# Optimization experiments

Hardware: AMD Instinct MI355X
Metric: run time of the kernel (lower is better)

The kernel has to match this reference:

```python
import jax, jax.numpy as jnp
import numpy as np

N, E, IN_DIM, HID, OUT = 50000, 800000, 256, 128, 128
EPS_BN = 1e-5
EPS_NORM = 1e-12


def leaky(x):
    return jnp.where(x >= 0, x, 0.2 * x)


def batchnorm(x, gamma, beta):
    # training-mode BatchNorm1d over node dimension
    mean = jnp.mean(x, axis=0)
    var = jnp.var(x, axis=0)
    return gamma * (x - mean) * jax.lax.rsqrt(var + EPS_BN) + beta


def sage_conv(x, src, dst, W_l, b_l, W_r):
    # PyG SAGEConv (mean aggr): lin_l(mean_{j->i} x_j) + lin_r(x_i)
    msg = x[src]  # [E, D] gather
    agg = jax.ops.segment_sum(msg, dst, num_segments=N)
    cnt = jax.ops.segment_sum(jnp.ones((E,), x.dtype), dst, num_segments=N)
    agg = agg / jnp.maximum(cnt, 1.0)[:, None]
    return agg @ W_l + b_l + x @ W_r


def setup_inputs() -> dict:
    key = jax.random.key(0)
    ks = jax.random.split(key, 16)
    s = lambda fan_in: (2.0 / fan_in) ** 0.5
    return {
        "x": jax.random.normal(ks[0], (N, IN_DIM), jnp.float32),
        "edge_index": jax.random.randint(ks[1], (2, E), 0, N),
        "W_in": jax.random.normal(ks[2], (IN_DIM, HID), jnp.float32) * s(IN_DIM),
        "b_in": jnp.zeros((HID,), jnp.float32),
        "g1": jnp.ones((HID,), jnp.float32),
        "be1": jnp.zeros((HID,), jnp.float32),
        "Wl1": jax.random.normal(ks[3], (HID, HID), jnp.float32) * s(HID),
        "bl1": jnp.zeros((HID,), jnp.float32),
        "Wr1": jax.random.normal(ks[4], (HID, HID), jnp.float32) * s(HID),
        "Wl2": jax.random.normal(ks[5], (HID, OUT), jnp.float32) * s(HID),
        "bl2": jnp.zeros((OUT,), jnp.float32),
        "Wr2": jax.random.normal(ks[6], (HID, OUT), jnp.float32) * s(HID),
        "Wskip": jax.random.normal(ks[7], (HID, OUT), jnp.float32) * s(HID),
        "bskip": jnp.zeros((OUT,), jnp.float32),
        "g2": jnp.ones((OUT,), jnp.float32),
        "be2": jnp.zeros((OUT,), jnp.float32),
    }


def reference(x, edge_index, W_in, b_in, g1, be1, Wl1, bl1, Wr1, Wl2, bl2, Wr2, Wskip, bskip, g2, be2):
    src, dst = edge_index[0], edge_index[1]
    h = batchnorm(leaky(x @ W_in + b_in), g1, be1)
    skip = h
    h1 = leaky(sage_conv(h, src, dst, Wl1, bl1, Wr1))  # dropout = identity (eval)
    h2 = sage_conv(h1, src, dst, Wl2, bl2, Wr2)
    out = h2 + (skip @ Wskip + bskip)
    out = batchnorm(out, g2, be2)
    norm = jnp.sqrt(jnp.sum(out * out, axis=1, keepdims=True))
    return out / jnp.maximum(norm, EPS_NORM)
```

## Files before the change

### kernel.cpp

```cpp
#include <hip/hip_runtime.h>
#include <math.h>

#define N_NODES 50000
#define N_EDGES 800000
#define IN_DIM 256
#define HID 128
#define ZPITCH 384

typedef unsigned short u16;
typedef u16 u16x8 __attribute__((ext_vector_type(8)));
typedef u16 u16x2 __attribute__((ext_vector_type(2)));
typedef __bf16 bf16x8 __attribute__((ext_vector_type(8)));
typedef float f32x4 __attribute__((ext_vector_type(4)));

union F8 { u16x8 u; bf16x8 h; };

__device__ __forceinline__ u16 f2b(float f) {
    unsigned u = __builtin_bit_cast(unsigned, f);
    u = (u + 0x7FFFu + ((u >> 16) & 1u)) >> 16;
    return (u16)u;
}
__device__ __forceinline__ float b2f(u16 h) {
    unsigned u = ((unsigned)h) << 16;
    return __builtin_bit_cast(float, u);
}

template<int A_F32>
__device__ __forceinline__ F8 load_a(const void* base, size_t row, int P, int koff)
{
    F8 r;
    if (A_F32) {
        const float* p = (const float*)base + row * P + koff;
        float4 f0 = *reinterpret_cast<const float4*>(p);
        float4 f1 = *reinterpret_cast<const float4*>(p + 4);
        r.h[0] = (__bf16)f0.x; r.h[1] = (__bf16)f0.y;
        r.h[2] = (__bf16)f0.z; r.h[3] = (__bf16)f0.w;
        r.h[4] = (__bf16)f1.x; r.h[5] = (__bf16)f1.y;
        r.h[6] = (__bf16)f1.z; r.h[7] = (__bf16)f1.w;
    } else {
        r.u = *reinterpret_cast<const u16x8*>((const u16*)base + row * P + koff);
    }
    return r;
}

template<int LEAKY, int STATS, int OUT_BF16, int A_F32, int NC>
__global__ __launch_bounds__(512, 3) void gemm_mfma(
    int M, const void* __restrict__ A, int P,
    const u16* __restrict__ Wf,
    const float* __restrict__ bias0, const float* __restrict__ bias1,
    void* __restrict__ Cout, int CP,
    float* __restrict__ stats)
{
    __shared__ u16 Bs[NC * 4096];

    const int t   = threadIdx.x;
    const int w   = t >> 6;
    const int l   = t & 63;
    const int l15 = l & 15;
    const int lg  = l >> 4;
    const int rb  = blockIdx.x * 128 + w * 16;

    int r0 = rb + l15;
    size_t r0c = (size_t)(r0 < M ? r0 : M - 1);
    const int ko = lg * 8;

    F8 a[NC];
#pragma unroll
    for (int c = 0; c < NC; ++c) a[c] = load_a<A_F32>(A, r0c, P, c * 32 + ko);

#pragma unroll
    for (int i = 0; i < NC; ++i) {
        int idx = i * 512 + t;
        reinterpret_cast<u16x8*>(Bs)[idx] = reinterpret_cast<const u16x8*>(Wf)[idx];
    }
    __syncthreads();

    f32x4 acc[8];
#pragma unroll
    for (int j = 0; j < 8; ++j) acc[j] = 0.0f;

#pragma unroll
    for (int c = 0; c < NC; ++c) {
#pragma unroll
        for (int j = 0; j < 8; ++j) {
            F8 b;
            b.u = reinterpret_cast<const u16x8*>(Bs)[(c * 8 + j) * 64 + l];
            acc[j] = __builtin_amdgcn_mfma_f32_16x16x32_bf16(a[c].h, b.h, acc[j], 0, 0, 0);
        }
    }

    float bias_j[8];
#pragma unroll
    for (int j = 0; j < 8; ++j) {
        float bb = bias0[16 * j + l15];
        if (bias1) bb += bias1[16 * j + l15];
        bias_j[j] = bb;
    }

    float csum[8], csq[8];
#pragma unroll
    for (int j = 0; j < 8; ++j) { csum[j] = 0.f; csq[j] = 0.f; }

    {
        int rbase = rb + lg * 4;
#pragma unroll
        for (int r = 0; r < 4; ++r) {
            int row = rbase + r;
            bool ok = row < M;
#pragma unroll
            for (int j = 0; j < 8; ++j) {
                float y = acc[j][r] + bias_j[j];
                if (LEAKY) y = (y >= 0.f) ? y : 0.2f * y;
                if (ok) {
                    if (OUT_BF16)
                        ((u16*)Cout)[(size_t)row * CP + 16 * j + l15] = f2b(y);
                    else
                        ((float*)Cout)[(size_t)row * CP + 16 * j + l15] = y;
                    if (STATS) { csum[j] += y; csq[j] += y * y; }
                }
            }
        }
    }

    if (STATS) {
        __shared__ float sred[256];
        if (t < 256) sred[t] = 0.f;
        __syncthreads();
#pragma unroll
        for (int j = 0; j < 8; ++j) {
            float s = csum[j];
            float q = csq[j];
            s += __shfl_xor(s, 16); s += __shfl_xor(s, 32);
            q += __shfl_xor(q, 16); q += __shfl_xor(q, 32);
            if (lg == 0) {
                atomicAdd(&sred[16 * j + l15], s);
                atomicAdd(&sred[128 + 16 * j + l15], q);
            }
        }
        __syncthreads();
        if (t < 256) atomicAdd(&stats[t], sred[t]);
    }
}

__global__ __launch_bounds__(256) void conv_w(const float* s0, const float* s1, const float* s2,
                                              const float* sc0, const float* sc1, const float* sc2,
                                              int rows_each, u16* __restrict__ dst, int nchunks)
{
    int tid = blockIdx.x * 256 + threadIdx.x;
    if (tid >= nchunks * 512) return;
    int c   = tid >> 9;
    int j   = (tid >> 6) & 7;
    int l   = tid & 63;
    int l15 = l & 15, lg = l >> 4;

    int srow0 = c * 32;
    int si    = srow0 / rows_each;
    const float* S  = (si == 0) ? s0 : (si == 1) ? s1 : s2;
    const float* SC = (si == 0) ? sc0 : (si == 1) ? sc1 : sc2;
    int rbase = srow0 - si * rows_each + lg * 8;
    int col   = 16 * j + l15;

    u16x8 o;
#pragma unroll
    for (int i = 0; i < 8; ++i) {
        float v = S[(size_t)(rbase + i) * HID + col];
        if (SC) v *= SC[rbase + i];
        o[i] = f2b(v);
    }
    reinterpret_cast<u16x8*>(dst)[tid] = o;
}

__global__ void bias_fold(const float* __restrict__ b0, const float* __restrict__ b1,
                          const float* __restrict__ W0, const float* __restrict__ W1,
                          const float* __restrict__ sh, float* __restrict__ outb)
{
    int j = threadIdx.x;
    float acc = b0[j] + (b1 ? b1[j] : 0.f);
    for (int i = 0; i < HID; ++i) {
        float w = W0[(size_t)i * HID + j] + (W1 ? W1[(size_t)i * HID + j] : 0.f);
        acc = fmaf(sh[i], w, acc);
    }
    outb[j] = acc;
}

__global__ void bn_params(const float* __restrict__ stats,
                          const float* __restrict__ gamma,
                          const float* __restrict__ beta,
                          float* __restrict__ scale,
                          float* __restrict__ shift, float invn)
{
    int j = threadIdx.x;
    float mean = stats[j] * invn;
    float var  = stats[128 + j] * invn - mean * mean;
    var = fmaxf(var, 0.f);
    float sc = gamma[j] / sqrtf(var + 1e-5f);
    scale[j] = sc;
    shift[j] = beta[j] - mean * sc;
}

__global__ __launch_bounds__(256) void edge_count(const int* __restrict__ dst, int* __restrict__ cnt)
{
    int e = blockIdx.x * 256 + threadIdx.x;
    if (e < N_EDGES) atomicAdd(&cnt[dst[e]], 1);
}

__global__ __launch_bounds__(256) void scan_block(const int* __restrict__ cnt,
                                                  int* __restrict__ excl,
                                                  int* __restrict__ bsum, int n)
{
    __shared__ int sh[256];
    int t = threadIdx.x;
    int i = blockIdx.x * 256 + t;
    int v = (i < n) ? cnt[i] : 0;
    sh[t] = v;
    __syncthreads();
#pragma unroll
    for (int off = 1; off < 256; off <<= 1) {
        int x = (t >= off) ? sh[t - off] : 0;
        __syncthreads();
        sh[t] += x;
        __syncthreads();
    }
    if (i < n) excl[i] = sh[t] - v;
    if (t == 255) bsum[blockIdx.x] = sh[255];
}

__global__ __launch_bounds__(256) void scan_bsum(int* __restrict__ bsum, int nb)
{
    __shared__ int sh[256];
    int t = threadIdx.x;
    int v = (t < nb) ? bsum[t] : 0;
    sh[t] = v;
    __syncthreads();
#pragma unroll
    for (int off = 1; off < 256; off <<= 1) {
        int x = (t >= off) ? sh[t - off] : 0;
        __syncthreads();
        sh[t] += x;
        __syncthreads();
    }
    if (t < nb) bsum[t] = sh[t] - v;
}

__global__ __launch_bounds__(256) void scan_add(int* __restrict__ row_ptr,
                                                int* __restrict__ fillrp,
                                                const int* __restrict__ bsum, int n)
{
    int i = blockIdx.x * 256 + threadIdx.x;
    if (i < n) {
        int v = row_ptr[i] + bsum[i >> 8];
        row_ptr[i] = v;
        fillrp[i]  = v;
    }
    if (i == 0) row_ptr[n] = N_EDGES;
}

#define FILL_EPB 4096
__global__ __launch_bounds__(256) void edge_fill_part(const int* __restrict__ src,
                                                      const int* __restrict__ dst,
                                                      int* __restrict__ fillrp,
                                                      int* __restrict__ col_idx)
{
    const int range = blockIdx.x & 7;
    const int base  = (blockIdx.x >> 3) * FILL_EPB;
    const int lo = range * 6250, hi = lo + 6250;
#pragma unroll
    for (int k = 0; k < FILL_EPB / 256; ++k) {
        int e = base + k * 256 + threadIdx.x;
        if (e < N_EDGES) {
            int d = dst[e];
            if (d >= lo && d < hi) {
                int pos = atomicAdd(&fillrp[d], 1);
                col_idx[pos] = src[e];
            }
        }
    }
}

__global__ __launch_bounds__(256) void spmm_mean(const int* __restrict__ row_ptr,
                                                 const int* __restrict__ col_idx,
                                                 const u16* __restrict__ Z_in,
                                                 u16* __restrict__ Z_out)
{
    int node = blockIdx.x * 4 + (threadIdx.x >> 6);
    if (node >= N_NODES) return;
    int lane = threadIdx.x & 63;
    int beg = row_ptr[node];
    int end = row_ptr[node + 1];

    float sx = 0.f, sy = 0.f;
    int e = beg;
    for (; e + 4 <= end; e += 4) {
        int c0 = col_idx[e], c1 = col_idx[e + 1], c2 = col_idx[e + 2], c3 = col_idx[e + 3];
        u16x2 v0 = *reinterpret_cast<const u16x2*>(Z_in + (size_t)c0 * ZPITCH + lane * 2);
        u16x2 v1 = *reinterpret_cast<const u16x2*>(Z_in + (size_t)c1 * ZPITCH + lane * 2);
        u16x2 v2 = *reinterpret_cast<const u16x2*>(Z_in + (size_t)c2 * ZPITCH + lane * 2);
        u16x2 v3 = *reinterpret_cast<const u16x2*>(Z_in + (size_t)c3 * ZPITCH + lane * 2);
        sx += (b2f(v0[0]) + b2f(v1[0])) + (b2f(v2[0]) + b2f(v3[0]));
        sy += (b2f(v0[1]) + b2f(v1[1])) + (b2f(v2[1]) + b2f(v3[1]));
    }
    for (; e < end; ++e) {
        int c = col_idx[e];
        u16x2 v = *reinterpret_cast<const u16x2*>(Z_in + (size_t)c * ZPITCH + lane * 2);
        sx += b2f(v[0]); sy += b2f(v[1]);
    }
    float inv = 1.f / fmaxf((float)(end - beg), 1.f);
    u16x2 r; r[0] = f2b(sx * inv); r[1] = f2b(sy * inv);
    *reinterpret_cast<u16x2*>(Z_out + (size_t)node * ZPITCH + lane * 2) = r;
}

__global__ __launch_bounds__(256) void bn_rownorm(float* __restrict__ out,
                                                  const float* __restrict__ scale,
                                                  const float* __restrict__ shift)
{
    int row = blockIdx.x * 4 + (threadIdx.x >> 6);
    if (row >= N_NODES) return;
    int lane = threadIdx.x & 63;
    float2 v  = *reinterpret_cast<const float2*>(&out[(size_t)row * HID + lane * 2]);
    float2 sc = *reinterpret_cast<const float2*>(&scale[lane * 2]);
    float2 sh = *reinterpret_cast<const float2*>(&shift[lane * 2]);
    float y0 = v.x * sc.x + sh.x;
    float y1 = v.y * sc.y + sh.y;
    float ss = y0 * y0 + y1 * y1;
#pragma unroll
    for (int m = 1; m < 64; m <<= 1) ss += __shfl_xor(ss, m);
    float inv = 1.f / fmaxf(sqrtf(ss), 1e-12f);
    float2 r = {y0 * inv, y1 * inv};
    *reinterpret_cast<float2*>(&out[(size_t)row * HID + lane * 2]) = r;
}

extern "C" void kernel_launch(void* const* d_in, const int* in_sizes, int n_in,
                              void* d_out, int out_size, void* d_ws, size_t ws_size,
                              hipStream_t stream)
{
    const float* x     = (const float*)d_in[0];
    const int*   ei    = (const int*)d_in[1];
    const float* W_in  = (const float*)d_in[2];
    const float* b_in  = (const float*)d_in[3];
    const float* g1    = (const float*)d_in[4];
    const float* be1   = (const float*)d_in[5];
    const float* Wl1   = (const float*)d_in[6];
    const float* bl1   = (const float*)d_in[7];
    const float* Wr1   = (const float*)d_in[8];
    const float* Wl2   = (const float*)d_in[9];
    const float* bl2   = (const float*)d_in[10];
    const float* Wr2   = (const float*)d_in[11];
    const float* Wskip = (const float*)d_in[12];
    const float* bskip = (const float*)d_in[13];
    const float* g2    = (const float*)d_in[14];
    const float* be2   = (const float*)d_in[15];
    float* out = (float*)d_out;

    char* ws = (char*)d_ws;
    u16*  Z  = (u16*)ws;
    char* zzone = ws + 38400000;
    float* stats = (float*)zzone;
    int*   icnt  = (int*)(zzone + 2048);
    size_t zsz   = 2048 + (size_t)N_NODES * 4;
    int*   row_ptr = (int*)(zzone + zsz);
    int*   fillrp  = (int*)(zzone + zsz + 200064);
    int*   bsum    = (int*)(zzone + zsz + 400128);
    int*   col_idx = (int*)(zzone + zsz + 400128 + 1024);
    float* bnc     = (float*)(zzone + zsz + 400128 + 1024 + (size_t)N_EDGES * 4);
    u16* WfA = (u16*)((char*)bnc + 4096);
    u16* WfB = WfA + 8 * 4096;
    u16* WfC = WfB + 8 * 4096;

    hipMemsetAsync(zzone, 0, zsz, stream);

    const int* srcp = ei;
    const int* dstp = ei + N_EDGES;

    float* scale1 = bnc;
    float* shift1 = bnc + 128;
    float* scale2 = bnc + 256;
    float* shift2 = bnc + 384;
    float* b1eff  = bnc + 512;
    float* b2eff  = bnc + 640;

    conv_w<<<16, 256, 0, stream>>>(W_in, nullptr, nullptr, nullptr, nullptr, nullptr,
                                   256, WfA, 8);

    const int NB = (N_NODES + 255) / 256;
    edge_count<<<(N_EDGES + 255) / 256, 256, 0, stream>>>(dstp, icnt);
    scan_block<<<NB, 256, 0, stream>>>(icnt, row_ptr, bsum, N_NODES);
    scan_bsum<<<1, 256, 0, stream>>>(bsum, NB);
    scan_add<<<NB, 256, 0, stream>>>(row_ptr, fillrp, bsum, N_NODES);
    edge_fill_part<<<((N_EDGES + FILL_EPB - 1) / FILL_EPB) * 8, 256, 0, stream>>>(
        srcp, dstp, fillrp, col_idx);

    const int GB = (N_NODES + 127) / 128;

    gemm_mfma<1, 1, 1, 1, 8><<<GB, 512, 0, stream>>>(
        N_NODES, x, IN_DIM, WfA, b_in, nullptr, Z + 128, ZPITCH, stats);
    bn_params<<<1, 128, 0, stream>>>(stats, g1, be1, scale1, shift1, 1.f / N_NODES);

    conv_w<<<16, 256, 0, stream>>>(Wl1, Wr1, nullptr, scale1, scale1, nullptr,
                                   128, WfB, 8);
    conv_w<<<24, 256, 0, stream>>>(Wl2, Wskip, Wr2, nullptr, scale1, nullptr,
                                   128, WfC, 12);
    bias_fold<<<1, 128, 0, stream>>>(bl1, nullptr, Wl1, Wr1, shift1, b1eff);
    bias_fold<<<1, 128, 0, stream>>>(bl2, bskip, Wskip, nullptr, shift1, b2eff);

    spmm_mean<<<(N_NODES + 3) / 4, 256, 0, stream>>>(row_ptr, col_idx, Z + 128, Z);
    gemm_mfma<1, 0, 1, 0, 8><<<GB, 512, 0, stream>>>(
        N_NODES, Z, ZPITCH, WfB, b1eff, nullptr, Z + 256, ZPITCH, nullptr);

    spmm_mean<<<(N_NODES + 3) / 4, 256, 0, stream>>>(row_ptr, col_idx, Z + 256, Z);
    gemm_mfma<0, 1, 0, 0, 12><<<GB, 512, 0, stream>>>(
        N_NODES, Z, ZPITCH, WfC, b2eff, nullptr, out, HID, stats + 256);

    bn_params<<<1, 128, 0, stream>>>(stats + 256, g2, be2, scale2, shift2, 1.f / N_NODES);
    bn_rownorm<<<(N_NODES + 3) / 4, 256, 0, stream>>>(out, scale2, shift2);
}
```

Before: 276.2 us.

## Fuse mean aggregation into SAGE GEMM kernels and restructure the launch pipeline

Replaces the separate spmm_mean plus gemm passes with sage_k kernels that gather neighbour means into LDS and immediately run the MFMA GEMM, so the aggregated features are never written to global memory. It also merges weight conversion with edge counting, applies BN1 explicitly to H instead of folding it into the weights and biases, and folds BN2 parameter computation into the row-norm kernel. The first GEMM now computes two 16-row tiles per wave and uses global_load_lds for weight staging. The cost is large 1024-thread blocks with heavy LDS use, which limits occupancy for the latency-bound gather, plus an extra bn_apply pass over H.

```diff
diff --git a/kernel.cpp b/kernel.cpp
--- a/kernel.cpp
+++ b/kernel.cpp
@@ -5,7 +5,7 @@
 #define N_EDGES 800000
 #define IN_DIM 256
 #define HID 128
-#define ZPITCH 384
+#define NTILE 196
 
 typedef unsigned short u16;
 typedef u16 u16x8 __attribute__((ext_vector_type(8)));
@@ -13,6 +13,9 @@
 typedef __bf16 bf16x8 __attribute__((ext_vector_type(8)));
 typedef float f32x4 __attribute__((ext_vector_type(4)));
 
+#define AS1 __attribute__((address_space(1)))
+#define AS3 __attribute__((address_space(3)))
+
 union F8 { u16x8 u; bf16x8 h; };
 
 __device__ __forceinline__ u16 f2b(float f) {
@@ -25,67 +28,342 @@
     return __builtin_bit_cast(float, u);
 }
 
-template<int A_F32>
-__device__ __forceinline__ F8 load_a(const void* base, size_t row, int P, int koff)
-{
-    F8 r;
-    if (A_F32) {
-        const float* p = (const float*)base + row * P + koff;
-        float4 f0 = *reinterpret_cast<const float4*>(p);
-        float4 f1 = *reinterpret_cast<const float4*>(p + 4);
-        r.h[0] = (__bf16)f0.x; r.h[1] = (__bf16)f0.y;
-        r.h[2] = (__bf16)f0.z; r.h[3] = (__bf16)f0.w;
-        r.h[4] = (__bf16)f1.x; r.h[5] = (__bf16)f1.y;
-        r.h[6] = (__bf16)f1.z; r.h[7] = (__bf16)f1.w;
+__device__ __forceinline__ void conv_seg(int tid, const float* s0, const float* s1,
+                                         const float* s2, int rows_each, u16* dst)
+{
+    int c   = tid >> 9;
+    int j   = (tid >> 6) & 7;
+    int l   = tid & 63;
+    int l15 = l & 15, lg = l >> 4;
+    int srow0 = c * 32;
+    int si    = srow0 / rows_each;
+    const float* S = (si == 0) ? s0 : (si == 1) ? s1 : s2;
+    int rbase = srow0 - si * rows_each + lg * 8;
+    int col   = 16 * j + l15;
+    u16x8 o;
+#pragma unroll
+    for (int i = 0; i < 8; ++i) o[i] = f2b(S[(size_t)(rbase + i) * HID + col]);
+    reinterpret_cast<u16x8*>(dst)[tid] = o;
+}
+
+__global__ __launch_bounds__(256) void convcnt_k(
+    const float* W_in, const float* Wl1, const float* Wr1,
+    const float* Wl2, const float* Wskip, const float* Wr2,
+    u16* WfA, u16* WfB, u16* WfC,
+    const int* __restrict__ dst, int* __restrict__ icnt)
+{
+    int b = blockIdx.x;
+    if (b < 56) {
+        int tid = b * 256 + threadIdx.x;
+        if (tid < 4096)      conv_seg(tid,        W_in, nullptr, nullptr, 256, WfA);
+        else if (tid < 8192) conv_seg(tid - 4096, Wl1,  Wr1,     nullptr, 128, WfB);
+        else                 conv_seg(tid - 8192, Wl2,  Wskip,   Wr2,     128, WfC);
     } else {
-        r.u = *reinterpret_cast<const u16x8*>((const u16*)base + row * P + koff);
-    }
-    return r;
-}
-
-template<int LEAKY, int STATS, int OUT_BF16, int A_F32, int NC>
-__global__ __launch_bounds__(512, 3) void gemm_mfma(
-    int M, const void* __restrict__ A, int P,
-    const u16* __restrict__ Wf,
-    const float* __restrict__ bias0, const float* __restrict__ bias1,
-    void* __restrict__ Cout, int CP,
+        int e = (b - 56) * 256 + threadIdx.x;
+        if (e < N_EDGES) atomicAdd(&icnt[dst[e]], 1);
+    }
+}
+
+__global__ __launch_bounds__(256) void scan_block(const int* __restrict__ cnt,
+                                                  int* __restrict__ excl,
+                                                  int* __restrict__ bsum, int n)
+{
+    __shared__ int sh[256];
+    int t = threadIdx.x;
+    int i = blockIdx.x * 256 + t;
+    int v = (i < n) ? cnt[i] : 0;
+    sh[t] = v;
+    __syncthreads();
+#pragma unroll
+    for (int off = 1; off < 256; off <<= 1) {
+        int x = (t >= off) ? sh[t - off] : 0;
+        __syncthreads();
+        sh[t] += x;
+        __syncthreads();
+    }
+    if (i < n) excl[i] = sh[t] - v;
+    if (t == 255) bsum[blockIdx.x] = sh[255];
+}
+
+__global__ __launch_bounds__(256) void scan_bsum(int* __restrict__ bsum, int nb)
+{
+    __shared__ int sh[256];
+    int t = threadIdx.x;
+    int v = (t < nb) ? bsum[t] : 0;
+    sh[t] = v;
+    __syncthreads();
+#pragma unroll
+    for (int off = 1; off < 256; off <<= 1) {
+        int x = (t >= off) ? sh[t - off] : 0;
+        __syncthreads();
+        sh[t] += x;
+        __syncthreads();
+    }
+    if (t < nb) bsum[t] = sh[t] - v;
+}
+
+__global__ __launch_bounds__(256) void scan_add(int* __restrict__ row_ptr,
+                                                int* __restrict__ fillrp,
+                                                const int* __restrict__ bsum, int n)
+{
+    int i = blockIdx.x * 256 + threadIdx.x;
+    if (i < n) {
+        int v = row_ptr[i] + bsum[i >> 8];
+        row_ptr[i] = v;
+        fillrp[i]  = v;
+    }
+    if (i == 0) row_ptr[n] = N_EDGES;
+}
+
+#define FILL_EPB 4096
+__global__ __launch_bounds__(256) void edge_fill_part(const int* __restrict__ src,
+                                                      const int* __restrict__ dst,
+                                                      int* __restrict__ fillrp,
+                                                      int* __restrict__ col_idx)
+{
+    const int range = blockIdx.x & 7;
+    const int base  = (blockIdx.x >> 3) * FILL_EPB;
+    const int lo = range * 6250, hi = lo + 6250;
+#pragma unroll
+    for (int k = 0; k < FILL_EPB / 256; ++k) {
+        int e = base + k * 256 + threadIdx.x;
+        if (e < N_EDGES) {
+            int d = dst[e];
+            if (d >= lo && d < hi) {
+                int pos = atomicAdd(&fillrp[d], 1);
+                col_idx[pos] = src[e];
+            }
+        }
+    }
+}
+
+__global__ __launch_bounds__(512, 2) void gemm0_k(
+    const float* __restrict__ x, const u16* __restrict__ Wf,
+    const float* __restrict__ bias, u16* __restrict__ H,
     float* __restrict__ stats)
 {
-    __shared__ u16 Bs[NC * 4096];
-
-    const int t   = threadIdx.x;
-    const int w   = t >> 6;
-    const int l   = t & 63;
-    const int l15 = l & 15;
-    const int lg  = l >> 4;
-    const int rb  = blockIdx.x * 128 + w * 16;
-
-    int r0 = rb + l15;
-    size_t r0c = (size_t)(r0 < M ? r0 : M - 1);
+    __shared__ u16 Bs[8 * 4096];
+    __shared__ float sred[256];
+    const int t = threadIdx.x, w = t >> 6, l = t & 63, l15 = l & 15, lg = l >> 4;
+    const int rb = blockIdx.x * 256 + w * 32;
+    const int r0 = rb + l15, r1 = r0 + 16;
+    const size_t r0c = (size_t)(r0 < N_NODES ? r0 : N_NODES - 1);
+    const size_t r1c = (size_t)(r1 < N_NODES ? r1 : N_NODES - 1);
     const int ko = lg * 8;
 
-    F8 a[NC];
-#pragma unroll
-    for (int c = 0; c < NC; ++c) a[c] = load_a<A_F32>(A, r0c, P, c * 32 + ko);
-
-#pragma unroll
-    for (int i = 0; i < NC; ++i) {
+#pragma unroll
+    for (int i = 0; i < 8; ++i) {
         int idx = i * 512 + t;
-        reinterpret_cast<u16x8*>(Bs)[idx] = reinterpret_cast<const u16x8*>(Wf)[idx];
-    }
-    __syncthreads();
-
-    f32x4 acc[8];
-#pragma unroll
-    for (int j = 0; j < 8; ++j) acc[j] = 0.0f;
-
-#pragma unroll
-    for (int c = 0; c < NC; ++c) {
+        __builtin_amdgcn_global_load_lds((const AS1 void*)(Wf + (size_t)idx * 8),
+                                         (AS3 void*)(Bs + (size_t)idx * 8), 16, 0, 0);
+    }
+    __syncthreads();
+
+    f32x4 acc[2][8];
+#pragma unroll
+    for (int m = 0; m < 2; ++m)
+#pragma unroll
+        for (int j = 0; j < 8; ++j) acc[m][j] = 0.0f;
+
+#pragma unroll
+    for (int c = 0; c < 8; ++c) {
+        F8 fa0, fa1;
+        {
+            const float* p = x + r0c * IN_DIM + c * 32 + ko;
+            float4 f0 = *reinterpret_cast<const float4*>(p);
+            float4 f1 = *reinterpret_cast<const float4*>(p + 4);
+            fa0.h[0] = (__bf16)f0.x; fa0.h[1] = (__bf16)f0.y;
+            fa0.h[2] = (__bf16)f0.z; fa0.h[3] = (__bf16)f0.w;
+            fa0.h[4] = (__bf16)f1.x; fa0.h[5] = (__bf16)f1.y;
+            fa0.h[6] = (__bf16)f1.z; fa0.h[7] = (__bf16)f1.w;
+        }
+        {
+            const float* p = x + r1c * IN_DIM + c * 32 + ko;
+            float4 f0 = *reinterpret_cast<const float4*>(p);
+            float4 f1 = *reinterpret_cast<const float4*>(p + 4);
+            fa1.h[0] = (__bf16)f0.x; fa1.h[1] = (__bf16)f0.y;
+            fa1.h[2] = (__bf16)f0.z; fa1.h[3] = (__bf16)f0.w;
+            fa1.h[4] = (__bf16)f1.x; fa1.h[5] = (__bf16)f1.y;
+            fa1.h[6] = (__bf16)f1.z; fa1.h[7] = (__bf16)f1.w;
+        }
 #pragma unroll
         for (int j = 0; j < 8; ++j) {
             F8 b;
-            b.u = reinterpret_cast<const u16x8*>(Bs)[(c * 8 + j) * 64 + l];
-            acc[j] = __builtin_amdgcn_mfma_f32_16x16x32_bf16(a[c].h, b.h, acc[j], 0, 0, 0);
+            b.u = *reinterpret_cast<const u16x8*>(Bs + (size_t)((c * 8 + j) * 64 + l) * 8);
+            acc[0][j] = __builtin_amdgcn_mfma_f32_16x16x32_bf16(fa0.h, b.h, acc[0][j], 0, 0, 0);
+            acc[1][j] = __builtin_amdgcn_mfma_f32_16x16x32_bf16(fa1.h, b.h, acc[1][j], 0, 0, 0);
+        }
+    }
+
+    float bias_j[8];
+#pragma unroll
+    for (int j = 0; j < 8; ++j) bias_j[j] = bias[16 * j + l15];
+
+    float csum[8], csq[8];
+#pragma unroll
+    for (int j = 0; j < 8; ++j) { csum[j] = 0.f; csq[j] = 0.f; }
+
+#pragma unroll
+    for (int m = 0; m < 2; ++m) {
+        int rbase = rb + m * 16 + lg * 4;
+#pragma unroll
+        for (int r = 0; r < 4; ++r) {
+            int row = rbase + r;
+            bool ok = row < N_NODES;
+#pragma unroll
+            for (int j = 0; j < 8; ++j) {
+                float y = acc[m][j][r] + bias_j[j];
+                y = (y >= 0.f) ? y : 0.2f * y;
+                if (ok) {
+                    H[(size_t)row * HID + 16 * j + l15] = f2b(y);
+                    csum[j] += y; csq[j] += y * y;
+                }
+            }
+        }
+    }
+
+    if (t < 256) sred[t] = 0.f;
+    __syncthreads();
+#pragma unroll
+    for (int j = 0; j < 8; ++j) {
+        float s = csum[j];
+        float q = csq[j];
+        s += __shfl_xor(s, 16); s += __shfl_xor(s, 32);
+        q += __shfl_xor(q, 16); q += __shfl_xor(q, 32);
+        if (lg == 0) {
+            atomicAdd(&sred[16 * j + l15], s);
+            atomicAdd(&sred[128 + 16 * j + l15], q);
+        }
+    }
+    __syncthreads();
+    if (t < 256) atomicAdd(&stats[t], sred[t]);
+}
+
+__global__ __launch_bounds__(256) void bn_apply_k(
+    u16* __restrict__ H, const float* __restrict__ stats,
+    const float* __restrict__ g1, const float* __restrict__ be1)
+{
+    __shared__ float sc[128], sh[128];
+    int t = threadIdx.x;
+    if (t < 128) {
+        float mean = stats[t] * (1.f / N_NODES);
+        float var  = fmaxf(stats[128 + t] * (1.f / N_NODES) - mean * mean, 0.f);
+        float s = g1[t] / sqrtf(var + 1e-5f);
+        sc[t] = s; sh[t] = be1[t] - mean * s;
+    }
+    __syncthreads();
+    int idx = blockIdx.x * 256 + t;
+    if (idx >= N_NODES * 16) return;
+    int g = (idx & 15) * 8;
+    u16x8 v = *reinterpret_cast<u16x8*>(H + (size_t)idx * 8);
+    u16x8 o;
+#pragma unroll
+    for (int e = 0; e < 8; ++e) o[e] = f2b(b2f(v[e]) * sc[g + e] + sh[g + e]);
+    *reinterpret_cast<u16x8*>(H + (size_t)idx * 8) = o;
+}
+
+template<int NC, int TWO_STAGE, int LEAKY, int STATS, int OUT_BF16>
+__global__ __launch_bounds__(1024, 4) void sage_k(
+    const int* __restrict__ row_ptr, const int* __restrict__ col_idx,
+    const u16* __restrict__ Gsrc, const u16* __restrict__ Aop1,
+    const u16* __restrict__ Aop2, const u16* __restrict__ Wf,
+    const float* __restrict__ bias0, const float* __restrict__ bias1,
+    void* __restrict__ Cout, float* __restrict__ stats)
+{
+    __shared__ u16 Bs[8 * 4096];
+    __shared__ u16 At[16 * 2048];
+    __shared__ float sred[256];
+
+    const int t = threadIdx.x, w = t >> 6, l = t & 63, l15 = l & 15, lg = l >> 4;
+    const int rb = blockIdx.x * 256 + w * 16;
+    const int r0 = rb + l15;
+    const size_t r0c = (size_t)(r0 < N_NODES ? r0 : N_NODES - 1);
+    const int ko = lg * 8;
+
+    for (int idx = t; idx < 8 * 512; idx += 1024)
+        __builtin_amdgcn_global_load_lds((const AS1 void*)(Wf + (size_t)idx * 8),
+                                         (AS3 void*)(Bs + (size_t)idx * 8), 16, 0, 0);
+
+    u16x8 av[4];
+#pragma unroll
+    for (int c = 0; c < 4; ++c)
+        av[c] = *reinterpret_cast<const u16x8*>(Aop1 + r0c * HID + c * 32 + ko);
+    u16x8 bv[4];
+    if (TWO_STAGE) {
+#pragma unroll
+        for (int c = 0; c < 4; ++c)
+            bv[c] = *reinterpret_cast<const u16x8*>(Aop2 + r0c * HID + c * 32 + ko);
+    }
+
+    u16* wbase = At + w * 2048;
+    for (int ni = 0; ni < 16; ++ni) {
+        int node = rb + ni;
+        float sx = 0.f, sy = 0.f, inv = 0.f;
+        if (node < N_NODES) {
+            int beg = row_ptr[node], end = row_ptr[node + 1];
+            int e = beg;
+            for (; e + 4 <= end; e += 4) {
+                int c0 = col_idx[e], c1 = col_idx[e + 1], c2 = col_idx[e + 2], c3 = col_idx[e + 3];
+                u16x2 v0 = *reinterpret_cast<const u16x2*>(Gsrc + (size_t)c0 * HID + l * 2);
+                u16x2 v1 = *reinterpret_cast<const u16x2*>(Gsrc + (size_t)c1 * HID + l * 2);
+                u16x2 v2 = *reinterpret_cast<const u16x2*>(Gsrc + (size_t)c2 * HID + l * 2);
+                u16x2 v3 = *reinterpret_cast<const u16x2*>(Gsrc + (size_t)c3 * HID + l * 2);
+                sx += (b2f(v0[0]) + b2f(v1[0])) + (b2f(v2[0]) + b2f(v3[0]));
+                sy += (b2f(v0[1]) + b2f(v1[1])) + (b2f(v2[1]) + b2f(v3[1]));
+            }
+            for (; e < end; ++e) {
+                int c = col_idx[e];
+                u16x2 v = *reinterpret_cast<const u16x2*>(Gsrc + (size_t)c * HID + l * 2);
+                sx += b2f(v[0]); sy += b2f(v[1]);
+            }
+            inv = 1.f / fmaxf((float)(end - beg), 1.f);
+        }
+        u16x2 rr; rr[0] = f2b(sx * inv); rr[1] = f2b(sy * inv);
+        *reinterpret_cast<u16x2*>(wbase + ni * 128 + (((l >> 2) ^ ni) & 15) * 8 + (l & 3) * 2) = rr;
+    }
+
+    __syncthreads();
+
+    f32x4 acc[8];
+#pragma unroll
+    for (int j = 0; j < 8; ++j) acc[j] = 0.0f;
+
+#pragma unroll
+    for (int c = 0; c < 4; ++c) {
+        F8 fa;
+        fa.u = *reinterpret_cast<const u16x8*>(wbase + l15 * 128 + (((c * 4 + lg) ^ l15) & 15) * 8);
+#pragma unroll
+        for (int j = 0; j < 8; ++j) {
+            F8 b;
+            b.u = *reinterpret_cast<const u16x8*>(Bs + (size_t)((c * 8 + j) * 64 + l) * 8);
+            acc[j] = __builtin_amdgcn_mfma_f32_16x16x32_bf16(fa.h, b.h, acc[j], 0, 0, 0);
+        }
+    }
+#pragma unroll
+    for (int c = 4; c < 8; ++c) {
+        F8 fa; fa.u = av[c - 4];
+#pragma unroll
+        for (int j = 0; j < 8; ++j) {
+            F8 b;
+            b.u = *reinterpret_cast<const u16x8*>(Bs + (size_t)((c * 8 + j) * 64 + l) * 8);
+            acc[j] = __builtin_amdgcn_mfma_f32_16x16x32_bf16(fa.h, b.h, acc[j], 0, 0, 0);
+        }
+    }
+    if (TWO_STAGE) {
+        __syncthreads();
+        for (int idx = t; idx < 4 * 512; idx += 1024)
+            __builtin_amdgcn_global_load_lds((const AS1 void*)(Wf + (size_t)(4096 + idx) * 8),
+                                             (AS3 void*)(At + (size_t)idx * 8), 16, 0, 0);
+        __syncthreads();
+#pragma unroll
+        for (int c = 8; c < 12; ++c) {
+            F8 fa; fa.u = bv[c - 8];
+#pragma unroll
+            for (int j = 0; j < 8; ++j) {
+                F8 b;
+                b.u = *reinterpret_cast<const u16x8*>(At + (size_t)(((c - 8) * 8 + j) * 64 + l) * 8);
+                acc[j] = __builtin_amdgcn_mfma_f32_16x16x32_bf16(fa.h, b.h, acc[j], 0, 0, 0);
+            }
         }
     }
 
@@ -101,29 +379,27 @@
 #pragma unroll
     for (int j = 0; j < 8; ++j) { csum[j] = 0.f; csq[j] = 0.f; }
 
-    {
-        int rbase = rb + lg * 4;
-#pragma unroll
-        for (int r = 0; r < 4; ++r) {
-            int row = rbase + r;
-            bool ok = row < M;
-#pragma unroll
-            for (int j = 0; j < 8; ++j) {
-                float y = acc[j][r] + bias_j[j];
-                if (LEAKY) y = (y >= 0.f) ? y : 0.2f * y;
-                if (ok) {
-                    if (OUT_BF16)
-                        ((u16*)Cout)[(size_t)row * CP + 16 * j + l15] = f2b(y);
-                    else
-                        ((float*)Cout)[(size_t)row * CP + 16 * j + l15] = y;
-                    if (STATS) { csum[j] += y; csq[j] += y * y; }
-                }
+    int rbase = rb + lg * 4;
+#pragma unroll
+    for (int r = 0; r < 4; ++r) {
+        int row = rbase + r;
+        bool ok = row < N_NODES;
+#pragma unroll
+        for (int j = 0; j < 8; ++j) {
+            float y = acc[j][r] + bias_j[j];
+            if (LEAKY) y = (y >= 0.f) ? y : 0.2f * y;
+            if (ok) {
+                if (OUT_BF16)
+                    ((u16*)Cout)[(size_t)row * HID + 16 * j + l15] = f2b(y);
+                else
+                    ((float*)Cout)[(size_t)row * HID + 16 * j + l15] = y;
+                if (STATS) { csum[j] += y; csq[j] += y * y; }
             }
         }
     }
 
     if (STATS) {
-        __shared__ float sred[256];
+        __syncthreads();
         if (t < 256) sred[t] = 0.f;
         __syncthreads();
 #pragma unroll
@@ -142,185 +418,25 @@
     }
 }
 
-__global__ __launch_bounds__(256) void conv_w(const float* s0, const float* s1, const float* s2,
-                                              const float* sc0, const float* sc1, const float* sc2,
-                                              int rows_each, u16* __restrict__ dst, int nchunks)
-{
-    int tid = blockIdx.x * 256 + threadIdx.x;
-    if (tid >= nchunks * 512) return;
-    int c   = tid >> 9;
-    int j   = (tid >> 6) & 7;
-    int l   = tid & 63;
-    int l15 = l & 15, lg = l >> 4;
-
-    int srow0 = c * 32;
-    int si    = srow0 / rows_each;
-    const float* S  = (si == 0) ? s0 : (si == 1) ? s1 : s2;
-    const float* SC = (si == 0) ? sc0 : (si == 1) ? sc1 : sc2;
-    int rbase = srow0 - si * rows_each + lg * 8;
-    int col   = 16 * j + l15;
-
-    u16x8 o;
-#pragma unroll
-    for (int i = 0; i < 8; ++i) {
-        float v = S[(size_t)(rbase + i) * HID + col];
-        if (SC) v *= SC[rbase + i];
-        o[i] = f2b(v);
-    }
-    reinterpret_cast<u16x8*>(dst)[tid] = o;
-}
-
-__global__ void bias_fold(const float* __restrict__ b0, const float* __restrict__ b1,
-                          const float* __restrict__ W0, const float* __restrict__ W1,
-                          const float* __restrict__ sh, float* __restrict__ outb)
-{
-    int j = threadIdx.x;
-    float acc = b0[j] + (b1 ? b1[j] : 0.f);
-    for (int i = 0; i < HID; ++i) {
-        float w = W0[(size_t)i * HID + j] + (W1 ? W1[(size_t)i * HID + j] : 0.f);
-        acc = fmaf(sh[i], w, acc);
-    }
-    outb[j] = acc;
-}
-
-__global__ void bn_params(const float* __restrict__ stats,
-                          const float* __restrict__ gamma,
-                          const float* __restrict__ beta,
-                          float* __restrict__ scale,
-                          float* __restrict__ shift, float invn)
-{
-    int j = threadIdx.x;
-    float mean = stats[j] * invn;
-    float var  = stats[128 + j] * invn - mean * mean;
-    var = fmaxf(var, 0.f);
-    float sc = gamma[j] / sqrtf(var + 1e-5f);
-    scale[j] = sc;
-    shift[j] = beta[j] - mean * sc;
-}
-
-__global__ __launch_bounds__(256) void edge_count(const int* __restrict__ dst, int* __restrict__ cnt)
-{
-    int e = blockIdx.x * 256 + threadIdx.x;
-    if (e < N_EDGES) atomicAdd(&cnt[dst[e]], 1);
-}
-
-__global__ __launch_bounds__(256) void scan_block(const int* __restrict__ cnt,
-                                                  int* __restrict__ excl,
-                                                  int* __restrict__ bsum, int n)
-{
-    __shared__ int sh[256];
+__global__ __launch_bounds__(256) void rownorm_k(
+    float* __restrict__ out, const float* __restrict__ stats2,
+    const float* __restrict__ g2, const float* __restrict__ be2)
+{
+    __shared__ float sc[128], sh[128];
     int t = threadIdx.x;
-    int i = blockIdx.x * 256 + t;
-    int v = (i < n) ? cnt[i] : 0;
-    sh[t] = v;
-    __syncthreads();
-#pragma unroll
-    for (int off = 1; off < 256; off <<= 1) {
-        int x = (t >= off) ? sh[t - off] : 0;
-        __syncthreads();
-        sh[t] += x;
-        __syncthreads();
-    }
-    if (i < n) excl[i] = sh[t] - v;
-    if (t == 255) bsum[blockIdx.x] = sh[255];
-}
-
-__global__ __launch_bounds__(256) void scan_bsum(int* __restrict__ bsum, int nb)
-{
-    __shared__ int sh[256];
-    int t = threadIdx.x;
-    int v = (t < nb) ? bsum[t] : 0;
-    sh[t] = v;
-    __syncthreads();
-#pragma unroll
-    for (int off = 1; off < 256; off <<= 1) {
-        int x = (t >= off) ? sh[t - off] : 0;
-        __syncthreads();
-        sh[t] += x;
-        __syncthreads();
-    }
-    if (t < nb) bsum[t] = sh[t] - v;
-}
-
-__global__ __launch_bounds__(256) void scan_add(int* __restrict__ row_ptr,
-                                                int* __restrict__ fillrp,
-                                                const int* __restrict__ bsum, int n)
-{
-    int i = blockIdx.x * 256 + threadIdx.x;
-    if (i < n) {
-        int v = row_ptr[i] + bsum[i >> 8];
-        row_ptr[i] = v;
-        fillrp[i]  = v;
-    }
-    if (i == 0) row_ptr[n] = N_EDGES;
-}
-
-#define FILL_EPB 4096
-__global__ __launch_bounds__(256) void edge_fill_part(const int* __restrict__ src,
-                                                      const int* __restrict__ dst,
-                                                      int* __restrict__ fillrp,
-                                                      int* __restrict__ col_idx)
-{
-    const int range = blockIdx.x & 7;
-    const int base  = (blockIdx.x >> 3) * FILL_EPB;
-    const int lo = range * 6250, hi = lo + 6250;
-#pragma unroll
-    for (int k = 0; k < FILL_EPB / 256; ++k) {
-        int e = base + k * 256 + threadIdx.x;
-        if (e < N_EDGES) {
-            int d = dst[e];
-            if (d >= lo && d < hi) {
-                int pos = atomicAdd(&fillrp[d], 1);
-                col_idx[pos] = src[e];
-            }
-        }
-    }
-}
-
-__global__ __launch_bounds__(256) void spmm_mean(const int* __restrict__ row_ptr,
-                                                 const int* __restrict__ col_idx,
-                                                 const u16* __restrict__ Z_in,
-                                                 u16* __restrict__ Z_out)
-{
-    int node = blockIdx.x * 4 + (threadIdx.x >> 6);
-    if (node >= N_NODES) return;
-    int lane = threadIdx.x & 63;
-    int beg = row_ptr[node];
-    int end = row_ptr[node + 1];
-
-    float sx = 0.f, sy = 0.f;
-    int e = beg;
-    for (; e + 4 <= end; e += 4) {
-        int c0 = col_idx[e], c1 = col_idx[e + 1], c2 = col_idx[e + 2], c3 = col_idx[e + 3];
-        u16x2 v0 = *reinterpret_cast<const u16x2*>(Z_in + (size_t)c0 * ZPITCH + lane * 2);
-        u16x2 v1 = *reinterpret_cast<const u16x2*>(Z_in + (size_t)c1 * ZPITCH + lane * 2);
-        u16x2 v2 = *reinterpret_cast<const u16x2*>(Z_in + (size_t)c2 * ZPITCH + lane * 2);
-        u16x2 v3 = *reinterpret_cast<const u16x2*>(Z_in + (size_t)c3 * ZPITCH + lane * 2);
-        sx += (b2f(v0[0]) + b2f(v1[0])) + (b2f(v2[0]) + b2f(v3[0]));
-        sy += (b2f(v0[1]) + b2f(v1[1])) + (b2f(v2[1]) + b2f(v3[1]));
-    }
-    for (; e < end; ++e) {
-        int c = col_idx[e];
-        u16x2 v = *reinterpret_cast<const u16x2*>(Z_in + (size_t)c * ZPITCH + lane * 2);
-        sx += b2f(v[0]); sy += b2f(v[1]);
-    }
-    float inv = 1.f / fmaxf((float)(end - beg), 1.f);
-    u16x2 r; r[0] = f2b(sx * inv); r[1] = f2b(sy * inv);
-    *reinterpret_cast<u16x2*>(Z_out + (size_t)node * ZPITCH + lane * 2) = r;
-}
-
-__global__ __launch_bounds__(256) void bn_rownorm(float* __restrict__ out,
-                                                  const float* __restrict__ scale,
-                                                  const float* __restrict__ shift)
-{
-    int row = blockIdx.x * 4 + (threadIdx.x >> 6);
+    if (t < 128) {
+        float mean = stats2[t] * (1.f / N_NODES);
+        float var  = fmaxf(stats2[128 + t] * (1.f / N_NODES) - mean * mean, 0.f);
+        float s = g2[t] / sqrtf(var + 1e-5f);
+        sc[t] = s; sh[t] = be2[t] - mean * s;
+    }
+    __syncthreads();
+    int row = blockIdx.x * 4 + (t >> 6);
     if (row >= N_NODES) return;
-    int lane = threadIdx.x & 63;
-    float2 v  = *reinterpret_cast<const float2*>(&out[(size_t)row * HID + lane * 2]);
-    float2 sc = *reinterpret_cast<const float2*>(&scale[lane * 2]);
-    float2 sh = *reinterpret_cast<const float2*>(&shift[lane * 2]);
-    float y0 = v.x * sc.x + sh.x;
-    float y1 = v.y * sc.y + sh.y;
+    int lane = t & 63;
+    float2 v = *reinterpret_cast<const float2*>(&out[(size_t)row * HID + lane * 2]);
+    float y0 = v.x * sc[lane * 2]     + sh[lane * 2];
+    float y1 = v.y * sc[lane * 2 + 1] + sh[lane * 2 + 1];
     float ss = y0 * y0 + y1 * y1;
 #pragma unroll
     for (int m = 1; m < 64; m <<= 1) ss += __shfl_xor(ss, m);
@@ -351,65 +467,44 @@
     const float* be2   = (const float*)d_in[15];
     float* out = (float*)d_out;
 
+    const size_t NB16 = (size_t)N_NODES * HID;
     char* ws = (char*)d_ws;
-    u16*  Z  = (u16*)ws;
-    char* zzone = ws + 38400000;
-    float* stats = (float*)zzone;
-    int*   icnt  = (int*)(zzone + 2048);
-    size_t zsz   = 2048 + (size_t)N_NODES * 4;
-    int*   row_ptr = (int*)(zzone + zsz);
-    int*   fillrp  = (int*)(zzone + zsz + 200064);
-    int*   bsum    = (int*)(zzone + zsz + 400128);
-    int*   col_idx = (int*)(zzone + zsz + 400128 + 1024);
-    float* bnc     = (float*)(zzone + zsz + 400128 + 1024 + (size_t)N_EDGES * 4);
-    u16* WfA = (u16*)((char*)bnc + 4096);
-    u16* WfB = WfA + 8 * 4096;
-    u16* WfC = WfB + 8 * 4096;
-
-    hipMemsetAsync(zzone, 0, zsz, stream);
+    u16* H  = (u16*)ws;
+    u16* H1 = H + NB16;
+    char* zz = ws + 2 * NB16 * 2;
+    float* stats  = (float*)zz;
+    int* icnt     = (int*)(zz + 2048);
+    size_t zsz    = 2048 + (size_t)N_NODES * 4;
+    int* row_ptr  = (int*)(zz + 202048);
+    int* fillrp   = (int*)(zz + 402112);
+    int* bsum     = (int*)(zz + 602176);
+    int* col_idx  = (int*)(zz + 603200);
+    u16* WfA      = (u16*)(zz + 603200 + (size_t)N_EDGES * 4);
+    u16* WfB      = WfA + 8 * 4096;
+    u16* WfC      = WfB + 8 * 4096;
+
+    hipMemsetAsync(zz, 0, zsz, stream);
 
     const int* srcp = ei;
     const int* dstp = ei + N_EDGES;
 
-    float* scale1 = bnc;
-    float* shift1 = bnc + 128;
-    float* scale2 = bnc + 256;
-    float* shift2 = bnc + 384;
-    float* b1eff  = bnc + 512;
-    float* b2eff  = bnc + 640;
-
-    conv_w<<<16, 256, 0, stream>>>(W_in, nullptr, nullptr, nullptr, nullptr, nullptr,
-                                   256, WfA, 8);
-
-    const int NB = (N_NODES + 255) / 256;
-    edge_count<<<(N_EDGES + 255) / 256, 256, 0, stream>>>(dstp, icnt);
-    scan_block<<<NB, 256, 0, stream>>>(icnt, row_ptr, bsum, N_NODES);
-    scan_bsum<<<1, 256, 0, stream>>>(bsum, NB);
-    scan_add<<<NB, 256, 0, stream>>>(row_ptr, fillrp, bsum, N_NODES);
+    convcnt_k<<<56 + (N_EDGES + 255) / 256, 256, 0, stream>>>(
+        W_in, Wl1, Wr1, Wl2, Wskip, Wr2, WfA, WfB, WfC, dstp, icnt);
+
+    scan_block<<<NTILE, 256, 0, stream>>>(icnt, row_ptr, bsum, N_NODES);
+    scan_bsum<<<1, 256, 0, stream>>>(bsum, NTILE);
+    scan_add<<<NTILE, 256, 0, stream>>>(row_ptr, fillrp, bsum, N_NODES);
     edge_fill_part<<<((N_EDGES + FILL_EPB - 1) / FILL_EPB) * 8, 256, 0, stream>>>(
         srcp, dstp, fillrp, col_idx);
 
-    const int GB = (N_NODES + 127) / 128;
-
-    gemm_mfma<1, 1, 1, 1, 8><<<GB, 512, 0, stream>>>(
-        N_NODES, x, IN_DIM, WfA, b_in, nullptr, Z + 128, ZPITCH, stats);
-    bn_params<<<1, 128, 0, stream>>>(stats, g1, be1, scale1, shift1, 1.f / N_NODES);
-
-    conv_w<<<16, 256, 0, stream>>>(Wl1, Wr1, nullptr, scale1, scale1, nullptr,
-                                   128, WfB, 8);
-    conv_w<<<24, 256, 0, stream>>>(Wl2, Wskip, Wr2, nullptr, scale1, nullptr,
-                                   128, WfC, 12);
-    bias_fold<<<1, 128, 0, stream>>>(bl1, nullptr, Wl1, Wr1, shift1, b1eff);
-    bias_fold<<<1, 128, 0, stream>>>(bl2, bskip, Wskip, nullptr, shift1, b2eff);
-
-    spmm_mean<<<(N_NODES + 3) / 4, 256, 0, stream>>>(row_ptr, col_idx, Z + 128, Z);
-    gemm_mfma<1, 0, 1, 0, 8><<<GB, 512, 0, stream>>>(
-        N_NODES, Z, ZPITCH, WfB, b1eff, nullptr, Z + 256, ZPITCH, nullptr);
-
-    spmm_mean<<<(N_NODES + 3) / 4, 256, 0, stream>>>(row_ptr, col_idx, Z + 256, Z);
-    gemm_mfma<0, 1, 0, 0, 12><<<GB, 512, 0, stream>>>(
-        N_NODES, Z, ZPITCH, WfC, b2eff, nullptr, out, HID, stats + 256);
-
-    bn_params<<<1, 128, 0, stream>>>(stats + 256, g2, be2, scale2, shift2, 1.f / N_NODES);
-    bn_rownorm<<<(N_NODES + 3) / 4, 256, 0, stream>>>(out, scale2, shift2);
-}
+    gemm0_k<<<NTILE, 512, 0, stream>>>(x, WfA, b_in, H, stats);
+    bn_apply_k<<<(N_NODES * 16 + 255) / 256, 256, 0, stream>>>(H, stats, g1, be1);
+
+    sage_k<8, 0, 1, 0, 1><<<NTILE, 1024, 0, stream>>>(
+        row_ptr, col_idx, H, H, nullptr, WfB, bl1, nullptr, H1, nullptr);
+
+    sage_k<12, 1, 0, 1, 0><<<NTILE, 1024, 0, stream>>>(
+        row_ptr, col_idx, H1, H, H1, WfC, bl2, bskip, out, stats + 256);
+
+    rownorm_k<<<(N_NODES + 3) / 4, 256, 0, stream>>>(out, stats + 256, g2, be2);
+}
```

Measured after the change: 294.0 us. +6.5%, slower.
